# Kernel optimization log

Hardware: AMD Instinct MI355X
Metric: run time of the kernel (lower is better)

## Reference

```python
import jax, jax.numpy as jnp
import numpy as np

B, N, HID, NSEG = 16, 2048, 32, 3


def _cdist(p):
    # p: [..., N, 3] -> pairwise L2 distances [..., N, N] (matmul expansion)
    sq = jnp.sum(p * p, axis=-1)
    d2 = sq[..., :, None] + sq[..., None, :] - 2.0 * jnp.einsum('...nd,...md->...nm', p, p)
    d2 = jnp.maximum(d2, 0.0)
    return jnp.where(d2 > 0, jnp.sqrt(jnp.maximum(d2, 1e-12)), 0.0)


def _rigid_t(alpha, trans, center, sz):
    # alpha, trans: [B, NSEG, 3]
    c, s = jnp.cos(alpha), jnp.sin(alpha)
    b, t, _ = trans.shape
    z = jnp.zeros((b, t), alpha.dtype)
    o = jnp.ones((b, t), alpha.dtype)
    X = jnp.stack([c[..., 0], -s[..., 0], z, s[..., 0], c[..., 0], z, z, z, o], 2).reshape(b, t, 3, 3)
    Y = jnp.stack([c[..., 1], z, s[..., 1], z, o, z, -s[..., 1], z, c[..., 1]], 2).reshape(b, t, 3, 3)
    Z = jnp.stack([o, z, z, z, c[..., 2], -s[..., 2], z, s[..., 2], c[..., 2]], 2).reshape(b, t, 3, 3)
    XYZ = jnp.einsum('btmn,btnk,btks->btms', X, Y, Z)
    eye = jnp.eye(3, dtype=alpha.dtype)
    T = trans * sz[None, None, :] + jnp.einsum('m,btms->bts', center, eye[None, None] - XYZ)
    return XYZ, T


def _forward(x, W1, b1, W2, b2, A, center, sz):
    Bc, _, Nc = x.shape
    pos = x[:, :3, :]                                   # [B, 3, N]
    h = jax.nn.relu(pos.reshape(Bc, 3 * Nc) @ W1.T + b1)
    z_l = jnp.tanh(h @ W2.T + b2).reshape(Bc, NSEG, 6)
    # Faithful to source: both angles and translation use z_l[:, :, 3:]
    alpha = jnp.pi * z_l[:, :, 3:]
    trans = z_l[:, :, 3:]
    R, T = _rigid_t(alpha, trans, center, sz)           # [B,NSEG,3,3], [B,NSEG,3]
    # per-point segment id (contiguous tessellation), static numpy
    seg = np.concatenate([np.zeros(20, np.int32), np.ones(20, np.int32), np.full(Nc - 40, 2, np.int32)])
    Rp = R[:, seg]                                      # [B, N, 3, 3]
    Tp = T[:, seg]                                      # [B, N, 3]
    # einsum('bkt,bkn->btn', R, x) applied per point (= R^T x + T)
    pos_t = jnp.einsum('bnkt,bkn->btn', Rp, pos) + Tp.transpose(0, 2, 1)
    colors = jax.nn.softmax(x[:, 3:6, :], axis=1)
    X_t = jnp.concatenate([pos_t, colors], axis=1)      # [B, 6, N]
    # regularizer: Frobenius norm of atlas-vs-transformed-input distance mismatch
    dA = _cdist(A[:3, :].T)                             # [N, N]
    dx = _cdist(pos.transpose(0, 2, 1))                 # [B, N, N]
    diff = dA[None] - dx
    reg = jnp.sqrt(jnp.sum(diff * diff, axis=(1, 2)))   # [B]
    return X_t, reg


def setup_inputs() -> dict:
    key = jax.random.key(0)
    ks = jax.random.split(key, 6)
    x = jax.random.normal(ks[0], (B, 6, N), jnp.float32)
    W1 = jax.random.normal(ks[1], (HID, 3 * N), jnp.float32) * 0.02
    b1 = jax.random.normal(ks[2], (HID,), jnp.float32) * 0.02
    W2 = jax.random.normal(ks[3], (6 * NSEG, HID), jnp.float32) * 0.02
    b2 = jax.random.normal(ks[4], (6 * NSEG,), jnp.float32) * 0.02
    A = jax.random.normal(ks[5], (6, N), jnp.float32)
    sz = jnp.array([256.0, 256.0, 64.0], jnp.float32)
    center = sz / 2.0
    return {"x": x, "W1": W1, "b1": b1, "W2": W2, "b2": b2, "A": A,
            "center": center, "sz": sz, "times": 1}


def reference(x, W1, b1, W2, b2, A, center, sz, times):
    # `times` is accepted but unused, as in the original forward
    return _forward(x, W1, b1, W2, b2, A, center, sz)
```

## Files before the change

### kernel.cpp

```cpp
#include <hip/hip_runtime.h>
#include <hip/hip_bf16.h>

#define NPTS 2048
#define BATCH 16
#define REG_BASE 196608

#define H_OFF    0
#define RT_OFF   512
#define MOM_OFF  1088
#define POSW_OFF 1280
#define AW_OFF   (POSW_OFF + 16*2048*4)
#define WS_FLOATS (AW_OFF + 2048*4)
#define WS_BYTES  ((size_t)WS_FLOATS * 4)


__global__ __launch_bounds__(256) void k_h(
    const float* __restrict__ x, const float* __restrict__ W1,
    const float* __restrict__ b1, float* __restrict__ out,
    float* __restrict__ ws)
{
    const int jg = blockIdx.x, b = blockIdx.y;
    const int t = threadIdx.x;
    const int j = jg * 8 + (t >> 5);
    const int l = t & 31;

    if (jg == 0 && b == 0) {
        if (t < BATCH) out[REG_BASE + t] = 0.f;
        if (t < 68) ws[MOM_OFF + t] = 0.f;
    }

    const float4* xb4 = reinterpret_cast<const float4*>(x + (size_t)b * 12288);
    const float4* wj4 = reinterpret_cast<const float4*>(W1 + (size_t)j * 6144);
    float dot = 0.f;
    #pragma unroll 4
    for (int k = l; k < 1536; k += 32) {
        float4 a = xb4[k];
        float4 w = wj4[k];
        dot += a.x * w.x + a.y * w.y + a.z * w.z + a.w * w.w;
    }
    dot += __shfl_xor(dot, 1, 32);
    dot += __shfl_xor(dot, 2, 32);
    dot += __shfl_xor(dot, 4, 32);
    dot += __shfl_xor(dot, 8, 32);
    dot += __shfl_xor(dot, 16, 32);
    if (l == 0) ws[H_OFF + b * 32 + j] = fmaxf(dot + b1[j], 0.f);
}

__global__ __launch_bounds__(64) void k_zr(
    const float* __restrict__ W2, const float* __restrict__ b2,
    const float* __restrict__ center, const float* __restrict__ sz,
    float* __restrict__ ws)
{
    const int t = threadIdx.x;
    if (t >= 48) return;
    const int b = t / 3, s = t % 3;
    const float* hb = ws + H_OFF + b * 32;

    float z[3];
    #pragma unroll
    for (int d = 0; d < 3; ++d) {
        const int row = s * 6 + 3 + d;
        float acc = b2[row];
        #pragma unroll
        for (int j = 0; j < 32; ++j) acc += hb[j] * W2[row * 32 + j];
        z[d] = tanhf(acc);
    }
    const float PI = 3.14159265358979323846f;
    float c0 = cosf(PI * z[0]), s0 = sinf(PI * z[0]);
    float c1 = cosf(PI * z[1]), s1 = sinf(PI * z[1]);
    float c2 = cosf(PI * z[2]), s2 = sinf(PI * z[2]);
    float X[3][3] = {{c0, -s0, 0.f}, {s0, c0, 0.f}, {0.f, 0.f, 1.f}};
    float Y[3][3] = {{c1, 0.f, s1}, {0.f, 1.f, 0.f}, {-s1, 0.f, c1}};
    float Z[3][3] = {{1.f, 0.f, 0.f}, {0.f, c2, -s2}, {0.f, s2, c2}};
    float YZ[3][3], M[3][3];
    for (int m = 0; m < 3; ++m)
        for (int n = 0; n < 3; ++n) {
            float v = 0.f;
            for (int k = 0; k < 3; ++k) v += Y[m][k] * Z[k][n];
            YZ[m][n] = v;
        }
    float* rt = ws + RT_OFF + (b * 3 + s) * 12;
    for (int m = 0; m < 3; ++m)
        for (int n = 0; n < 3; ++n) {
            float v = 0.f;
            for (int k = 0; k < 3; ++k) v += X[m][k] * YZ[k][n];
            M[m][n] = v;
            rt[m * 3 + n] = v;
        }
    for (int d = 0; d < 3; ++d)
        rt[9 + d] = z[d] * sz[d] + center[d]
                  - (center[0] * M[0][d] + center[1] * M[1][d] + center[2] * M[2][d]);
}

__global__ __launch_bounds__(256) void k_transform(
    const float* __restrict__ x, const float* __restrict__ A,
    float* __restrict__ out, float* __restrict__ ws)
{
    const int c = blockIdx.x, b = blockIdx.y;
    const int t = threadIdx.x;
    const int n = c * 256 + t;
    float4* posw = reinterpret_cast<float4*>(ws + POSW_OFF);
    float4* aw   = reinterpret_cast<float4*>(ws + AW_OFF);

    float px, py, pz;
    if (b < BATCH) {
        const float* xb = x + (size_t)b * 12288;
        px = xb[n]; py = xb[2048 + n]; pz = xb[4096 + n];
        posw[b * 2048 + n] = make_float4(px, py, pz, 0.f);

        const int s = (n < 20) ? 0 : (n < 40) ? 1 : 2;
        const float* rt = ws + RT_OFF + (b * 3 + s) * 12;
        float* ob = out + (size_t)b * 12288;
        #pragma unroll
        for (int d = 0; d < 3; ++d)
            ob[d * 2048 + n] = rt[0 * 3 + d] * px + rt[1 * 3 + d] * py
                             + rt[2 * 3 + d] * pz + rt[9 + d];

        float c3 = xb[6144 + n], c4 = xb[8192 + n], c5 = xb[10240 + n];
        float mx = fmaxf(c3, fmaxf(c4, c5));
        float e3 = __expf(c3 - mx), e4 = __expf(c4 - mx), e5 = __expf(c5 - mx);
        float inv = 1.f / (e3 + e4 + e5);
        ob[6144 + n] = e3 * inv;
        ob[8192 + n] = e4 * inv;
        ob[10240 + n] = e5 * inv;
    } else {
        px = A[n]; py = A[2048 + n]; pz = A[4096 + n];
        aw[n] = make_float4(px, py, pz, 0.f);
    }

    float v0 = px, v1 = py, v2 = pz, v3 = px * px + py * py + pz * pz;
    #pragma unroll
    for (int m = 1; m < 64; m <<= 1) {
        v0 += __shfl_xor(v0, m);
        v1 += __shfl_xor(v1, m);
        v2 += __shfl_xor(v2, m);
        v3 += __shfl_xor(v3, m);
    }
    __shared__ float wpart[4][4];
    const int w = t >> 6;
    if ((t & 63) == 0) {
        wpart[w][0] = v0; wpart[w][1] = v1; wpart[w][2] = v2; wpart[w][3] = v3;
    }
    __syncthreads();
    if (t < 4) {
        float s4 = wpart[0][t] + wpart[1][t] + wpart[2][t] + wpart[3][t];
        atomicAdd(&ws[MOM_OFF + b * 4 + t], s4);
    }
}

__global__ __launch_bounds__(256) void k_reg_s(
    const float* __restrict__ ws_ro, float* __restrict__ out)
{
    const int bx = blockIdx.x, b = blockIdx.y;
    const int p = bx >> 1, h = bx & 1;
    int ci = 0, rem = p;
    while (rem >= 8 - ci) { rem -= 8 - ci; ++ci; }
    const int cj = ci + rem;
    const int t = threadIdx.x;

    const float4* posw = reinterpret_cast<const float4*>(ws_ro + POSW_OFF);
    const float4* aw   = reinterpret_cast<const float4*>(ws_ro + AW_OFF);

    const int i = ci * 256 + t;
    const int jb = cj * 256 + h * 128;
    float4 Pi = posw[(size_t)b * 2048 + i];
    float4 Ai = aw[i];
    const float pix = Pi.x, piy = Pi.y, piz = Pi.z;
    const float aix = Ai.x, aiy = Ai.y, aiz = Ai.z;

    const float4* pj = posw + (size_t)b * 2048 + jb;
    const float4* aj = aw + jb;

    float a0 = 0.f, a1 = 0.f, a2 = 0.f, a3 = 0.f;

#define PAIR_BODY(K, ACC, PRED)                                          \
    {                                                                    \
        float4 P = pj[jj + K];                                           \
        float4 Q = aj[jj + K];                                           \
        float ux = pix - P.x, uy = piy - P.y, uz = piz - P.z;            \
        float d2x = ux * ux + uy * uy + uz * uz;                         \
        float vx = aix - Q.x, vy = aiy - Q.y, vz = aiz - Q.z;            \
        float d2a = vx * vx + vy * vy + vz * vz;                         \
        float s = __builtin_amdgcn_sqrtf(d2x * d2a);                     \
        if (PRED) s = (jb + jj + K > i) ? s : 0.f;                       \
        ACC += s;                                                        \
    }

    if (ci != cj) {
        for (int jj = 0; jj < 128; jj += 4) {
            PAIR_BODY(0, a0, false)
            PAIR_BODY(1, a1, false)
            PAIR_BODY(2, a2, false)
            PAIR_BODY(3, a3, false)
        }
    } else {
        for (int jj = 0; jj < 128; jj += 4) {
            PAIR_BODY(0, a0, true)
            PAIR_BODY(1, a1, true)
            PAIR_BODY(2, a2, true)
            PAIR_BODY(3, a3, true)
        }
    }
#undef PAIR_BODY

    float acc = (a0 + a1) + (a2 + a3);
    #pragma unroll
    for (int m = 1; m < 64; m <<= 1) acc += __shfl_xor(acc, m);
    __shared__ float wsum[4];
    if ((t & 63) == 0) wsum[t >> 6] = acc;
    __syncthreads();
    if (t == 0)
        atomicAdd(&out[REG_BASE + b], wsum[0] + wsum[1] + wsum[2] + wsum[3]);
}

__global__ void k_final_s(float* __restrict__ out, const float* __restrict__ ws)
{
    const int b = threadIdx.x;
    if (b >= BATCH) return;
    const float* ma = ws + MOM_OFF + 16 * 4;
    const float* mb = ws + MOM_OFF + b * 4;
    float S2a = 2.f * (2048.f * ma[3] - (ma[0]*ma[0] + ma[1]*ma[1] + ma[2]*ma[2]));
    float S2x = 2.f * (2048.f * mb[3] - (mb[0]*mb[0] + mb[1]*mb[1] + mb[2]*mb[2]));
    float cross = out[REG_BASE + b];
    out[REG_BASE + b] = sqrtf(fmaxf(S2a + S2x - 4.f * cross, 0.f));
}

__global__ __launch_bounds__(256) void k_mlp_fb(
    const float* __restrict__ x, const float* __restrict__ W1,
    const float* __restrict__ b1, const float* __restrict__ W2,
    const float* __restrict__ b2, const float* __restrict__ center,
    const float* __restrict__ sz, float* __restrict__ out)
{
    const int b = blockIdx.x;
    const int t = threadIdx.x;
    __shared__ float hbuf[32];
    __shared__ float zbuf[18];
    __shared__ float Rl[3][9];
    __shared__ float Tl[3][3];
    {
        const int j = t >> 3;
        const int l = t & 7;
        const float4* xb4 = reinterpret_cast<const float4*>(x + (size_t)b * 12288);
        const float4* wj4 = reinterpret_cast<const float4*>(W1 + (size_t)j * 6144);
        float dot = 0.f;
        #pragma unroll 4
        for (int k = l; k < 1536; k += 8) {
            float4 a = xb4[k];
            float4 w = wj4[k];
            dot += a.x * w.x + a.y * w.y + a.z * w.z + a.w * w.w;
        }
        dot += __shfl_xor(dot, 1);
        dot += __shfl_xor(dot, 2);
        dot += __shfl_xor(dot, 4);
        if (l == 0) hbuf[j] = fmaxf(dot + b1[j], 0.f);
    }
    if (t == 0) out[REG_BASE + b] = 0.f;
    __syncthreads();
    if (t < 18) {
        float s = b2[t];
        #pragma unroll
        for (int j = 0; j < 32; ++j) s += hbuf[j] * W2[t * 32 + j];
        zbuf[t] = tanhf(s);
    }
    __syncthreads();
    if (t < 3) {
        const int s = t;
        const float PI = 3.14159265358979323846f;
        float a0 = PI * zbuf[s * 6 + 3], a1 = PI * zbuf[s * 6 + 4], a2 = PI * zbuf[s * 6 + 5];
        float c0 = cosf(a0), s0 = sinf(a0);
        float c1 = cosf(a1), s1 = sinf(a1);
        float c2 = cosf(a2), s2 = sinf(a2);
        float X[3][3] = {{c0, -s0, 0.f}, {s0, c0, 0.f}, {0.f, 0.f, 1.f}};
        float Y[3][3] = {{c1, 0.f, s1}, {0.f, 1.f, 0.f}, {-s1, 0.f, c1}};
        float Z[3][3] = {{1.f, 0.f, 0.f}, {0.f, c2, -s2}, {0.f, s2, c2}};
        float YZ[3][3], M[3][3];
        for (int m = 0; m < 3; ++m)
            for (int n = 0; n < 3; ++n) {
                float v = 0.f;
                for (int k = 0; k < 3; ++k) v += Y[m][k] * Z[k][n];
                YZ[m][n] = v;
            }
        for (int m = 0; m < 3; ++m)
            for (int n = 0; n < 3; ++n) {
                float v = 0.f;
                for (int k = 0; k < 3; ++k) v += X[m][k] * YZ[k][n];
                M[m][n] = v;
                Rl[s][m * 3 + n] = v;
            }
        for (int sd = 0; sd < 3; ++sd)
            Tl[s][sd] = zbuf[s * 6 + 3 + sd] * sz[sd] + center[sd]
                      - (center[0] * M[0][sd] + center[1] * M[1][sd] + center[2] * M[2][sd]);
    }
    __syncthreads();
    const float* xb = x + (size_t)b * 12288;
    float* ob = out + (size_t)b * 12288;
    for (int n = t; n < 2048; n += 256) {
        float px = xb[n], py = xb[2048 + n], pz = xb[4096 + n];
        int s = (n < 20) ? 0 : (n < 40) ? 1 : 2;
        #pragma unroll
        for (int td = 0; td < 3; ++td)
            ob[td * 2048 + n] = Rl[s][0 * 3 + td] * px + Rl[s][1 * 3 + td] * py
                              + Rl[s][2 * 3 + td] * pz + Tl[s][td];
        float c3 = xb[6144 + n], c4 = xb[8192 + n], c5 = xb[10240 + n];
        float mx = fmaxf(c3, fmaxf(c4, c5));
        float e3 = __expf(c3 - mx), e4 = __expf(c4 - mx), e5 = __expf(c5 - mx);
        float inv = 1.f / (e3 + e4 + e5);
        ob[6144 + n] = e3 * inv;
        ob[8192 + n] = e4 * inv;
        ob[10240 + n] = e5 * inv;
    }
}

__global__ __launch_bounds__(256) void k_reg_fb(
    const float* __restrict__ x, const float* __restrict__ A,
    float* __restrict__ out)
{
    const int p = blockIdx.x;
    const int b = blockIdx.y;
    int ci = 0, rem = p;
    while (rem >= 8 - ci) { rem -= 8 - ci; ++ci; }
    const int cj = ci + rem;
    const int t = threadIdx.x;
    __shared__ float4 pj[256];
    __shared__ float4 aj[256];
    const float* xb = x + (size_t)b * 12288;
    {
        int j = cj * 256 + t;
        pj[t] = make_float4(xb[j], xb[2048 + j], xb[4096 + j], 0.f);
        aj[t] = make_float4(A[j], A[2048 + j], A[4096 + j], 0.f);
    }
    __syncthreads();
    const int i = ci * 256 + t;
    const float pix = xb[i], piy = xb[2048 + i], piz = xb[4096 + i];
    const float aix = A[i], aiy = A[2048 + i], aiz = A[4096 + i];
    const int jbase = cj * 256;
    float acc = 0.f;
    #pragma unroll 4
    for (int jj = 0; jj < 256; ++jj) {
        float4 P = pj[jj];
        float4 Q = aj[jj];
        float dx0 = pix - P.x, dy0 = piy - P.y, dz0 = piz - P.z;
        float dxv = sqrtf(dx0 * dx0 + dy0 * dy0 + dz0 * dz0);
        float da0 = aix - Q.x, da1 = aiy - Q.y, da2 = aiz - Q.z;
        float dav = sqrtf(da0 * da0 + da1 * da1 + da2 * da2);
        float d = dav - dxv;
        float dd = (jbase + jj > i) ? d : 0.f;
        acc = fmaf(dd, dd, acc);
    }
    #pragma unroll
    for (int m = 1; m < 64; m <<= 1) acc += __shfl_xor(acc, m);
    __shared__ float wsum[4];
    if ((t & 63) == 0) wsum[t >> 6] = acc;
    __syncthreads();
    if (t == 0) atomicAdd(&out[REG_BASE + b], wsum[0] + wsum[1] + wsum[2] + wsum[3]);
}

__global__ void k_final_fb(float* __restrict__ out)
{
    int b = threadIdx.x;
    if (b < BATCH) out[REG_BASE + b] = sqrtf(2.f * out[REG_BASE + b]);
}

extern "C" void kernel_launch(void* const* d_in, const int* in_sizes, int n_in,
                              void* d_out, int out_size, void* d_ws, size_t ws_size,
                              hipStream_t stream) {
    (void)in_sizes; (void)n_in; (void)out_size;
    const float* x      = (const float*)d_in[0];
    const float* W1     = (const float*)d_in[1];
    const float* b1     = (const float*)d_in[2];
    const float* W2     = (const float*)d_in[3];
    const float* b2     = (const float*)d_in[4];
    const float* A      = (const float*)d_in[5];
    const float* center = (const float*)d_in[6];
    const float* sz     = (const float*)d_in[7];
    float* out = (float*)d_out;
    float* ws  = (float*)d_ws;

    if (ws_size >= WS_BYTES) {
        k_h<<<dim3(4, 16), 256, 0, stream>>>(x, W1, b1, out, ws);
        k_zr<<<1, 64, 0, stream>>>(W2, b2, center, sz, ws);
        k_transform<<<dim3(8, 17), 256, 0, stream>>>(x, A, out, ws);
        k_reg_s<<<dim3(72, 16), 256, 0, stream>>>(ws, out);
        k_final_s<<<1, 64, 0, stream>>>(out, ws);
    } else {
        k_mlp_fb<<<BATCH, 256, 0, stream>>>(x, W1, b1, W2, b2, center, sz, out);
        k_reg_fb<<<dim3(36, 16), 256, 0, stream>>>(x, A, out);
        k_final_fb<<<1, 64, 0, stream>>>(out);
    }
}
```

Baseline: 107.4 us.

## Fuse rigid-param and final kernels, batch-tile cross term with readlane broadcast

Moves the tiny rigid-transform computation into each k_transform block, which drops the k_zr launch. The pairwise cross-term kernel now processes 4 batches per block so each atlas distance is reused across them, and it broadcasts j points with readlane instead of reloading from memory. The k_final launch is replaced by a last-block-done atomic counter that computes the final sqrt. This cuts launches and memory traffic, but each k_transform block now redundantly computes the MLP head and adds a serial tail in the last cross block.

```diff
diff --git a/kernel.cpp b/kernel.cpp
--- a/kernel.cpp
+++ b/kernel.cpp
@@ -5,29 +5,33 @@
 #define BATCH 16
 #define REG_BASE 196608
 
-#define H_OFF    0
-#define RT_OFF   512
-#define MOM_OFF  1088
-#define POSW_OFF 1280
-#define AW_OFF   (POSW_OFF + 16*2048*4)
+#define H_OFF     0
+#define MOM_OFF   512
+#define CROSS_OFF 580
+#define CNT_OFF   596
+#define POSW_OFF  640
+#define AW_OFF    (POSW_OFF + 16*2048*4)
 #define WS_FLOATS (AW_OFF + 2048*4)
 #define WS_BYTES  ((size_t)WS_FLOATS * 4)
 
+#define CBLKS 576
+
+__device__ __forceinline__ float rl(float v, int k) {
+    return __int_as_float(__builtin_amdgcn_readlane(__float_as_int(v), k));
+}
+
 
 __global__ __launch_bounds__(256) void k_h(
     const float* __restrict__ x, const float* __restrict__ W1,
-    const float* __restrict__ b1, float* __restrict__ out,
-    float* __restrict__ ws)
+    const float* __restrict__ b1, float* __restrict__ ws)
 {
     const int jg = blockIdx.x, b = blockIdx.y;
     const int t = threadIdx.x;
     const int j = jg * 8 + (t >> 5);
     const int l = t & 31;
 
-    if (jg == 0 && b == 0) {
-        if (t < BATCH) out[REG_BASE + t] = 0.f;
-        if (t < 68) ws[MOM_OFF + t] = 0.f;
-    }
+    if (jg == 0 && b == 0 && t < 85)
+        ws[MOM_OFF + t] = 0.f;
 
     const float4* xb4 = reinterpret_cast<const float4*>(x + (size_t)b * 12288);
     const float4* wj4 = reinterpret_cast<const float4*>(W1 + (size_t)j * 6144);
@@ -46,54 +50,10 @@
     if (l == 0) ws[H_OFF + b * 32 + j] = fmaxf(dot + b1[j], 0.f);
 }
 
-__global__ __launch_bounds__(64) void k_zr(
+__global__ __launch_bounds__(256) void k_transform(
+    const float* __restrict__ x, const float* __restrict__ A,
     const float* __restrict__ W2, const float* __restrict__ b2,
     const float* __restrict__ center, const float* __restrict__ sz,
-    float* __restrict__ ws)
-{
-    const int t = threadIdx.x;
-    if (t >= 48) return;
-    const int b = t / 3, s = t % 3;
-    const float* hb = ws + H_OFF + b * 32;
-
-    float z[3];
-    #pragma unroll
-    for (int d = 0; d < 3; ++d) {
-        const int row = s * 6 + 3 + d;
-        float acc = b2[row];
-        #pragma unroll
-        for (int j = 0; j < 32; ++j) acc += hb[j] * W2[row * 32 + j];
-        z[d] = tanhf(acc);
-    }
-    const float PI = 3.14159265358979323846f;
-    float c0 = cosf(PI * z[0]), s0 = sinf(PI * z[0]);
-    float c1 = cosf(PI * z[1]), s1 = sinf(PI * z[1]);
-    float c2 = cosf(PI * z[2]), s2 = sinf(PI * z[2]);
-    float X[3][3] = {{c0, -s0, 0.f}, {s0, c0, 0.f}, {0.f, 0.f, 1.f}};
-    float Y[3][3] = {{c1, 0.f, s1}, {0.f, 1.f, 0.f}, {-s1, 0.f, c1}};
-    float Z[3][3] = {{1.f, 0.f, 0.f}, {0.f, c2, -s2}, {0.f, s2, c2}};
-    float YZ[3][3], M[3][3];
-    for (int m = 0; m < 3; ++m)
-        for (int n = 0; n < 3; ++n) {
-            float v = 0.f;
-            for (int k = 0; k < 3; ++k) v += Y[m][k] * Z[k][n];
-            YZ[m][n] = v;
-        }
-    float* rt = ws + RT_OFF + (b * 3 + s) * 12;
-    for (int m = 0; m < 3; ++m)
-        for (int n = 0; n < 3; ++n) {
-            float v = 0.f;
-            for (int k = 0; k < 3; ++k) v += X[m][k] * YZ[k][n];
-            M[m][n] = v;
-            rt[m * 3 + n] = v;
-        }
-    for (int d = 0; d < 3; ++d)
-        rt[9 + d] = z[d] * sz[d] + center[d]
-                  - (center[0] * M[0][d] + center[1] * M[1][d] + center[2] * M[2][d]);
-}
-
-__global__ __launch_bounds__(256) void k_transform(
-    const float* __restrict__ x, const float* __restrict__ A,
     float* __restrict__ out, float* __restrict__ ws)
 {
     const int c = blockIdx.x, b = blockIdx.y;
@@ -102,19 +62,61 @@
     float4* posw = reinterpret_cast<float4*>(ws + POSW_OFF);
     float4* aw   = reinterpret_cast<float4*>(ws + AW_OFF);
 
+    __shared__ float zs[3][3];
+    __shared__ float Rl[3][9];
+    __shared__ float Tl[3][3];
+
     float px, py, pz;
     if (b < BATCH) {
+        if (t < 9) {
+            const int s = t / 3, d = t % 3;
+            const float* hb = ws + H_OFF + b * 32;
+            const int row = s * 6 + 3 + d;
+            float acc = b2[row];
+            #pragma unroll
+            for (int jj = 0; jj < 32; ++jj) acc += hb[jj] * W2[row * 32 + jj];
+            zs[s][d] = tanhf(acc);
+        }
+        __syncthreads();
+        if (t < 3) {
+            const int s = t;
+            const float PI = 3.14159265358979323846f;
+            float c0 = cosf(PI * zs[s][0]), s0 = sinf(PI * zs[s][0]);
+            float c1 = cosf(PI * zs[s][1]), s1 = sinf(PI * zs[s][1]);
+            float c2 = cosf(PI * zs[s][2]), s2 = sinf(PI * zs[s][2]);
+            float X[3][3] = {{c0, -s0, 0.f}, {s0, c0, 0.f}, {0.f, 0.f, 1.f}};
+            float Y[3][3] = {{c1, 0.f, s1}, {0.f, 1.f, 0.f}, {-s1, 0.f, c1}};
+            float Z[3][3] = {{1.f, 0.f, 0.f}, {0.f, c2, -s2}, {0.f, s2, c2}};
+            float YZ[3][3], M[3][3];
+            for (int m = 0; m < 3; ++m)
+                for (int nn = 0; nn < 3; ++nn) {
+                    float v = 0.f;
+                    for (int k = 0; k < 3; ++k) v += Y[m][k] * Z[k][nn];
+                    YZ[m][nn] = v;
+                }
+            for (int m = 0; m < 3; ++m)
+                for (int nn = 0; nn < 3; ++nn) {
+                    float v = 0.f;
+                    for (int k = 0; k < 3; ++k) v += X[m][k] * YZ[k][nn];
+                    M[m][nn] = v;
+                    Rl[s][m * 3 + nn] = v;
+                }
+            for (int d = 0; d < 3; ++d)
+                Tl[s][d] = zs[s][d] * sz[d] + center[d]
+                         - (center[0] * M[0][d] + center[1] * M[1][d] + center[2] * M[2][d]);
+        }
+        __syncthreads();
+
         const float* xb = x + (size_t)b * 12288;
         px = xb[n]; py = xb[2048 + n]; pz = xb[4096 + n];
         posw[b * 2048 + n] = make_float4(px, py, pz, 0.f);
 
         const int s = (n < 20) ? 0 : (n < 40) ? 1 : 2;
-        const float* rt = ws + RT_OFF + (b * 3 + s) * 12;
         float* ob = out + (size_t)b * 12288;
         #pragma unroll
         for (int d = 0; d < 3; ++d)
-            ob[d * 2048 + n] = rt[0 * 3 + d] * px + rt[1 * 3 + d] * py
-                             + rt[2 * 3 + d] * pz + rt[9 + d];
+            ob[d * 2048 + n] = Rl[s][0 * 3 + d] * px + Rl[s][1 * 3 + d] * py
+                             + Rl[s][2 * 3 + d] * pz + Tl[s][d];
 
         float c3 = xb[6144 + n], c4 = xb[8192 + n], c5 = xb[10240 + n];
         float mx = fmaxf(c3, fmaxf(c4, c5));
@@ -148,81 +150,104 @@
     }
 }
 
-__global__ __launch_bounds__(256) void k_reg_s(
-    const float* __restrict__ ws_ro, float* __restrict__ out)
-{
-    const int bx = blockIdx.x, b = blockIdx.y;
-    const int p = bx >> 1, h = bx & 1;
-    int ci = 0, rem = p;
-    while (rem >= 8 - ci) { rem -= 8 - ci; ++ci; }
-    const int cj = ci + rem;
+__global__ __launch_bounds__(256) void k_cross(
+    float* __restrict__ ws, float* __restrict__ out)
+{
+    const int bx = blockIdx.x;
+    const int tile = bx % 144;
+    const int b0 = (bx / 144) * 4;
+    int rem = tile, ci = 0;
+    while (rem >= 32 - 4 * ci) { rem -= 32 - 4 * ci; ++ci; }
+    const int cj = 4 * ci + rem;
     const int t = threadIdx.x;
-
-    const float4* posw = reinterpret_cast<const float4*>(ws_ro + POSW_OFF);
-    const float4* aw   = reinterpret_cast<const float4*>(ws_ro + AW_OFF);
-
+    const int ln = t & 63;
     const int i = ci * 256 + t;
-    const int jb = cj * 256 + h * 128;
-    float4 Pi = posw[(size_t)b * 2048 + i];
-    float4 Ai = aw[i];
-    const float pix = Pi.x, piy = Pi.y, piz = Pi.z;
-    const float aix = Ai.x, aiy = Ai.y, aiz = Ai.z;
-
-    const float4* pj = posw + (size_t)b * 2048 + jb;
-    const float4* aj = aw + jb;
+    const int jb = cj * 64;
+
+    const float4* posw = reinterpret_cast<const float4*>(ws + POSW_OFF);
+    const float4* aw   = reinterpret_cast<const float4*>(ws + AW_OFF);
+
+    const float4 Ai  = aw[i];
+    const float4 Aj  = aw[jb + ln];
+    const float4 Pi0 = posw[(size_t)(b0 + 0) * 2048 + i];
+    const float4 Pi1 = posw[(size_t)(b0 + 1) * 2048 + i];
+    const float4 Pi2 = posw[(size_t)(b0 + 2) * 2048 + i];
+    const float4 Pi3 = posw[(size_t)(b0 + 3) * 2048 + i];
+    const float4 Pj0 = posw[(size_t)(b0 + 0) * 2048 + jb + ln];
+    const float4 Pj1 = posw[(size_t)(b0 + 1) * 2048 + jb + ln];
+    const float4 Pj2 = posw[(size_t)(b0 + 2) * 2048 + jb + ln];
+    const float4 Pj3 = posw[(size_t)(b0 + 3) * 2048 + jb + ln];
 
     float a0 = 0.f, a1 = 0.f, a2 = 0.f, a3 = 0.f;
 
-#define PAIR_BODY(K, ACC, PRED)                                          \
-    {                                                                    \
-        float4 P = pj[jj + K];                                           \
-        float4 Q = aj[jj + K];                                           \
-        float ux = pix - P.x, uy = piy - P.y, uz = piz - P.z;            \
-        float d2x = ux * ux + uy * uy + uz * uz;                         \
-        float vx = aix - Q.x, vy = aiy - Q.y, vz = aiz - Q.z;            \
-        float d2a = vx * vx + vy * vy + vz * vz;                         \
-        float s = __builtin_amdgcn_sqrtf(d2x * d2a);                     \
-        if (PRED) s = (jb + jj + K > i) ? s : 0.f;                       \
-        ACC += s;                                                        \
-    }
-
-    if (ci != cj) {
-        for (int jj = 0; jj < 128; jj += 4) {
-            PAIR_BODY(0, a0, false)
-            PAIR_BODY(1, a1, false)
-            PAIR_BODY(2, a2, false)
-            PAIR_BODY(3, a3, false)
+#define CROSS_ONE(PI, PJ, ACC)                                              \
+    {                                                                       \
+        float ux = PI.x - rl(PJ.x, k);                                      \
+        float uy = PI.y - rl(PJ.y, k);                                      \
+        float uz = PI.z - rl(PJ.z, k);                                      \
+        float d2x = ux * ux + uy * uy + uz * uz;                            \
+        float s = __builtin_amdgcn_sqrtf(d2x * d2a);                        \
+        if (PRED) s = (jb + k > i) ? s : 0.f;                               \
+        ACC += s;                                                           \
+    }
+#define CROSS_STEP                                                          \
+    {                                                                       \
+        float qx = rl(Aj.x, k), qy = rl(Aj.y, k), qz = rl(Aj.z, k);         \
+        float vx = Ai.x - qx, vy = Ai.y - qy, vz = Ai.z - qz;               \
+        float d2a = vx * vx + vy * vy + vz * vz;                            \
+        CROSS_ONE(Pi0, Pj0, a0)                                             \
+        CROSS_ONE(Pi1, Pj1, a1)                                             \
+        CROSS_ONE(Pi2, Pj2, a2)                                             \
+        CROSS_ONE(Pi3, Pj3, a3)                                             \
+    }
+
+    if (rem < 4) {
+        #define PRED true
+        #pragma unroll 8
+        for (int k = 0; k < 64; ++k) CROSS_STEP
+        #undef PRED
+    } else {
+        #define PRED false
+        #pragma unroll 8
+        for (int k = 0; k < 64; ++k) CROSS_STEP
+        #undef PRED
+    }
+#undef CROSS_STEP
+#undef CROSS_ONE
+
+    #pragma unroll
+    for (int m = 1; m < 64; m <<= 1) {
+        a0 += __shfl_xor(a0, m);
+        a1 += __shfl_xor(a1, m);
+        a2 += __shfl_xor(a2, m);
+        a3 += __shfl_xor(a3, m);
+    }
+    __shared__ float wsum[4][4];
+    if (ln == 0) {
+        const int w = t >> 6;
+        wsum[w][0] = a0; wsum[w][1] = a1; wsum[w][2] = a2; wsum[w][3] = a3;
+    }
+    __syncthreads();
+    if (t == 0) {
+        #pragma unroll
+        for (int q = 0; q < 4; ++q) {
+            float s = wsum[0][q] + wsum[1][q] + wsum[2][q] + wsum[3][q];
+            atomicAdd(&ws[CROSS_OFF + b0 + q], s);
         }
-    } else {
-        for (int jj = 0; jj < 128; jj += 4) {
-            PAIR_BODY(0, a0, true)
-            PAIR_BODY(1, a1, true)
-            PAIR_BODY(2, a2, true)
-            PAIR_BODY(3, a3, true)
+        __threadfence();
+        unsigned old = atomicAdd(reinterpret_cast<unsigned*>(&ws[CNT_OFF]), 1u);
+        if (old == CBLKS - 1) {
+            __threadfence();
+            const float* ma = ws + MOM_OFF + 16 * 4;
+            float S2a = 2.f * (2048.f * ma[3] - (ma[0]*ma[0] + ma[1]*ma[1] + ma[2]*ma[2]));
+            for (int b = 0; b < BATCH; ++b) {
+                const float* mb = ws + MOM_OFF + b * 4;
+                float S2x = 2.f * (2048.f * mb[3] - (mb[0]*mb[0] + mb[1]*mb[1] + mb[2]*mb[2]));
+                float cr = atomicAdd(&ws[CROSS_OFF + b], 0.f);
+                out[REG_BASE + b] = sqrtf(fmaxf(S2a + S2x - 4.f * cr, 0.f));
+            }
         }
     }
-#undef PAIR_BODY
-
-    float acc = (a0 + a1) + (a2 + a3);
-    #pragma unroll
-    for (int m = 1; m < 64; m <<= 1) acc += __shfl_xor(acc, m);
-    __shared__ float wsum[4];
-    if ((t & 63) == 0) wsum[t >> 6] = acc;
-    __syncthreads();
-    if (t == 0)
-        atomicAdd(&out[REG_BASE + b], wsum[0] + wsum[1] + wsum[2] + wsum[3]);
-}
-
-__global__ void k_final_s(float* __restrict__ out, const float* __restrict__ ws)
-{
-    const int b = threadIdx.x;
-    if (b >= BATCH) return;
-    const float* ma = ws + MOM_OFF + 16 * 4;
-    const float* mb = ws + MOM_OFF + b * 4;
-    float S2a = 2.f * (2048.f * ma[3] - (ma[0]*ma[0] + ma[1]*ma[1] + ma[2]*ma[2]));
-    float S2x = 2.f * (2048.f * mb[3] - (mb[0]*mb[0] + mb[1]*mb[1] + mb[2]*mb[2]));
-    float cross = out[REG_BASE + b];
-    out[REG_BASE + b] = sqrtf(fmaxf(S2a + S2x - 4.f * cross, 0.f));
 }
 
 __global__ __launch_bounds__(256) void k_mlp_fb(
@@ -377,11 +402,9 @@
     float* ws  = (float*)d_ws;
 
     if (ws_size >= WS_BYTES) {
-        k_h<<<dim3(4, 16), 256, 0, stream>>>(x, W1, b1, out, ws);
-        k_zr<<<1, 64, 0, stream>>>(W2, b2, center, sz, ws);
-        k_transform<<<dim3(8, 17), 256, 0, stream>>>(x, A, out, ws);
-        k_reg_s<<<dim3(72, 16), 256, 0, stream>>>(ws, out);
-        k_final_s<<<1, 64, 0, stream>>>(out, ws);
+        k_h<<<dim3(4, 16), 256, 0, stream>>>(x, W1, b1, ws);
+        k_transform<<<dim3(8, 17), 256, 0, stream>>>(x, A, W2, b2, center, sz, out, ws);
+        k_cross<<<CBLKS, 256, 0, stream>>>(ws, out);
     } else {
         k_mlp_fb<<<BATCH, 256, 0, stream>>>(x, W1, b1, W2, b2, center, sz, out);
         k_reg_fb<<<dim3(36, 16), 256, 0, stream>>>(x, A, out);
```

Result: slower. 122.8 us (+14.3%).
